# Kernel optimization log

Measured on AMD Instinct MI355X. Metric: run time of the kernel, lower is better.

The kernel has to match this reference:

```python
import jax, jax.numpy as jnp
import numpy as np

N_NODES = 50000
N_EDGES = 800000
F_IN = 128
HID = 128
HID4 = HID // 4  # 32
N_SEL = 8192


def gcn_conv(x, src, dst, norm, W, b, n_nodes):
    h = x @ W                              # [N, out]
    msg = h[src] * norm[:, None]           # gather + scale, [E+N, out]
    out = jax.ops.segment_sum(msg, dst, num_segments=n_nodes)  # scatter-add
    return out + b


def setup_inputs() -> dict:
    key = jax.random.key(0)
    ks = jax.random.split(key, 12)
    def glorot(k, shape):
        lim = np.sqrt(6.0 / (shape[0] + shape[1])).astype(np.float32)
        return jax.random.uniform(k, shape, jnp.float32, -lim, lim)
    return {
        "x": jax.random.normal(ks[0], (N_NODES, F_IN), jnp.float32),
        "edge_index": jax.random.randint(ks[1], (2, N_EDGES), 0, N_NODES, jnp.int64 if jax.config.jax_enable_x64 else jnp.int32),
        "relevant_batch_indices": jax.random.randint(ks[2], (N_SEL,), 0, N_NODES),
        "labels": jax.random.randint(ks[3], (N_SEL,), 0, 2),
        "W1": glorot(ks[4], (F_IN, HID)),   "b1": jnp.zeros((HID,), jnp.float32),
        "W2": glorot(ks[5], (HID, HID4)),   "b2": jnp.zeros((HID4,), jnp.float32),
        "W3": glorot(ks[6], (HID4, HID4)),  "b3": jnp.zeros((HID4,), jnp.float32),
        "Wl": glorot(ks[7], (HID4, 2)),     "bl": jnp.zeros((2,), jnp.float32),
    }


def reference(x, edge_index, relevant_batch_indices, labels, W1, b1, W2, b2, W3, b3, Wl, bl):
    n = x.shape[0]
    loops = jnp.arange(n, dtype=edge_index.dtype)
    src = jnp.concatenate([edge_index[0], loops])  # add self-loops
    dst = jnp.concatenate([edge_index[1], loops])
    deg = jax.ops.segment_sum(jnp.ones_like(dst, dtype=x.dtype), dst, num_segments=n)
    dis = jnp.where(deg > 0, jax.lax.rsqrt(jnp.maximum(deg, 1e-12)), 0.0)
    norm = dis[src] * dis[dst]             # [E+N]

    h = jax.nn.relu(gcn_conv(x, src, dst, norm, W1, b1, n))
    h = jax.nn.relu(gcn_conv(h, src, dst, norm, W2, b2, n))
    h = gcn_conv(h, src, dst, norm, W3, b3, n)

    logits = h[relevant_batch_indices] @ Wl + bl   # [N_SEL, 2]
    softmax_vals = jax.nn.softmax(logits, axis=1)
    lsm = jax.nn.log_softmax(logits, axis=1)
    # original slices lsm to labels length if longer; here shapes match
    lsm = lsm[: labels.shape[0]]
    return (lsm, softmax_vals)
```

## Files before the change

### kernel.cpp

```cpp
#include <hip/hip_runtime.h>
#include <hip/hip_fp16.h>

#define F_IN 128
#define HID 128
#define HID4 32
#define NPB 256
#define SRC_BITS 17
#define NBK 256
#define MAXBUCKET 256

static inline size_t alignup(size_t x) { return (x + 255) & ~(size_t)255; }

typedef _Float16 half8 __attribute__((ext_vector_type(8)));
typedef float f32x4 __attribute__((ext_vector_type(4)));

union F4H8 { float4 f; __half2 h[4]; };
union U2H4 { uint2 u; _Float16 h[4]; };
union UH2  { unsigned u; __half2 h; };


__global__ __launch_bounds__(1024) void hist_k(const int* __restrict__ dst,
                                               int* __restrict__ ghist,
                                               const float* __restrict__ W1,
                                               _Float16* __restrict__ Wt,
                                               int ne, int n_buckets) {
    __shared__ int h[MAXBUCKET];
    const int t = threadIdx.x;
    if (blockIdx.x < 16) {
        int q = blockIdx.x * 1024 + t;
        int k = q >> 7, n = q & 127;
        Wt[n * 128 + k] = (_Float16)W1[q];
    }
    for (int b = t; b < n_buckets; b += 1024) h[b] = 0;
    __syncthreads();
    const int chunk = (ne + NBK - 1) / NBK;
    const int beg = blockIdx.x * chunk;
    const int end = min(ne, beg + chunk);
    for (int e = beg + t; e < end; e += 1024)
        atomicAdd(&h[dst[e] / NPB], 1);
    __syncthreads();
    for (int b = t; b < n_buckets; b += 1024)
        ghist[(size_t)b * NBK + blockIdx.x] = h[b];
}


__global__ void scan_block_k(const int* __restrict__ in, int* __restrict__ out,
                             int* __restrict__ partials, int n) {
    __shared__ int tmp[256];
    int i = blockIdx.x * 256 + threadIdx.x;
    int v = (i < n) ? in[i] : 0;
    tmp[threadIdx.x] = v;
    __syncthreads();
    for (int off = 1; off < 256; off <<= 1) {
        int t = (threadIdx.x >= off) ? tmp[threadIdx.x - off] : 0;
        __syncthreads();
        tmp[threadIdx.x] += t;
        __syncthreads();
    }
    if (i < n) out[i] = tmp[threadIdx.x] - v;
    if (threadIdx.x == 255) partials[blockIdx.x] = tmp[255];
}

__global__ void scan_partials_k(int* __restrict__ partials, int nb) {
    __shared__ int tmp[256];
    int v = (threadIdx.x < nb) ? partials[threadIdx.x] : 0;
    tmp[threadIdx.x] = v;
    __syncthreads();
    for (int off = 1; off < 256; off <<= 1) {
        int t = (threadIdx.x >= off) ? tmp[threadIdx.x - off] : 0;
        __syncthreads();
        tmp[threadIdx.x] += t;
        __syncthreads();
    }
    if (threadIdx.x < nb) partials[threadIdx.x] = tmp[threadIdx.x] - v;
}


__global__ __launch_bounds__(1024) void scatter2_k(const int* __restrict__ src, const int* __restrict__ dst,
                                                   const int* __restrict__ goff,
                                                   const int* __restrict__ partial2,
                                                   unsigned* __restrict__ tmp, int ne, int n_buckets) {
    __shared__ int cur[MAXBUCKET];
    const int t = threadIdx.x;
    for (int b = t; b < n_buckets; b += 1024)
        cur[b] = goff[(size_t)b * NBK + blockIdx.x] + partial2[b];
    __syncthreads();
    const int chunk = (ne + NBK - 1) / NBK;
    const int beg = blockIdx.x * chunk;
    const int end = min(ne, beg + chunk);
    for (int e = beg + t; e < end; e += 1024) {
        int d = dst[e];
        int s = src[e];
        int pos = atomicAdd(&cur[d / NPB], 1);
        tmp[pos] = ((unsigned)(d & (NPB - 1)) << SRC_BITS) | (unsigned)s;
    }
}


__global__ __launch_bounds__(NPB) void binC_k(const unsigned* __restrict__ tmp,
                                              const int* __restrict__ goff,
                                              const int* __restrict__ partial2,
                                              int* __restrict__ deg, float* __restrict__ dis,
                                              int* __restrict__ rowoff, int* __restrict__ csr,
                                              int n_nodes, int ne, int n_buckets) {
    __shared__ int cnt[NPB];
    __shared__ int sc[NPB];
    const int t = threadIdx.x;
    const int bid = blockIdx.x;
    const int base = goff[(size_t)bid * NBK] + partial2[bid];
    const int end = (bid + 1 < n_buckets) ? goff[(size_t)(bid + 1) * NBK] + partial2[bid + 1] : ne;

    cnt[t] = 0;
    __syncthreads();
    for (int j = base + t; j < end; j += NPB)
        atomicAdd(&cnt[tmp[j] >> SRC_BITS], 1);
    __syncthreads();

    int mydeg = cnt[t];
    sc[t] = mydeg;
    __syncthreads();
    for (int off = 1; off < NPB; off <<= 1) {
        int v = (t >= off) ? sc[t - off] : 0;
        __syncthreads();
        sc[t] += v;
        __syncthreads();
    }
    int excl = sc[t] - mydeg;
    int node = bid * NPB + t;
    if (node < n_nodes) {
        deg[node] = mydeg;
        dis[node] = rsqrtf((float)(mydeg + 1));
        rowoff[node] = base + excl;
    }
    cnt[t] = base + excl;
    __syncthreads();
    for (int j = base + t; j < end; j += NPB) {
        unsigned e = tmp[j];
        int ld = e >> SRC_BITS;
        int s  = e & ((1u << SRC_BITS) - 1);
        int pos = atomicAdd(&cnt[ld], 1);
        csr[pos] = s;
    }
}


__global__ __launch_bounds__(256) void gemm1_mfma_k(const float* __restrict__ in,
                                                    const _Float16* __restrict__ Wt,
                                                    const float* __restrict__ dis,
                                                    __half* __restrict__ hout, int n_rows) {
    __shared__ _Float16 xs[64][136];
    const int t = threadIdx.x;
    const int row0 = blockIdx.x * 64;

    #pragma unroll
    for (int i = 0; i < 8; ++i) {
        int q = t + i * 256;
        int row = q >> 5, c4 = (q & 31) * 4;
        float4 v = make_float4(0.f, 0.f, 0.f, 0.f);
        if (row0 + row < n_rows) v = *(const float4*)(in + (size_t)(row0 + row) * 128 + c4);
        U2H4 cv;
        cv.h[0] = (_Float16)v.x; cv.h[1] = (_Float16)v.y;
        cv.h[2] = (_Float16)v.z; cv.h[3] = (_Float16)v.w;
        *(uint2*)&xs[row][c4] = cv.u;
    }
    __syncthreads();

    const int lane = t & 63;
    const int wave = t >> 6;
    const int r0 = wave * 16;
    const int lrow = lane & 15;
    const int kgrp = (lane >> 4) * 8;

    f32x4 acc[8];
    #pragma unroll
    for (int c = 0; c < 8; ++c) acc[c] = (f32x4){0.f, 0.f, 0.f, 0.f};

    #pragma unroll
    for (int kk = 0; kk < 4; ++kk) {
        const int k0 = kk * 32 + kgrp;
        half8 a = *(const half8*)&xs[r0 + lrow][k0];
        #pragma unroll
        for (int ct = 0; ct < 8; ++ct) {
            half8 b = *(const half8*)(Wt + (size_t)(ct * 16 + lrow) * 128 + k0);
            acc[ct] = __builtin_amdgcn_mfma_f32_16x16x32_f16(a, b, acc[ct], 0, 0, 0);
        }
    }

    const int rbase = row0 + r0 + (lane >> 4) * 4;
    #pragma unroll
    for (int i = 0; i < 4; ++i) {
        int row = rbase + i;
        if (row < n_rows) {
            float sc = dis[row];
            __half* p = hout + (size_t)row * 128 + lrow;
            #pragma unroll
            for (int ct = 0; ct < 8; ++ct)
                p[ct * 16] = __float2half(sc * acc[ct][i]);
        }
    }
}


__global__ void pull1_k(const __half* __restrict__ g, const int* __restrict__ rowoff,
                        const int* __restrict__ deg, const int* __restrict__ csr,
                        const float* __restrict__ dis, const float* __restrict__ b,
                        float* __restrict__ out, int n_nodes) {
    int gt = blockIdx.x * blockDim.x + threadIdx.x;
    int node = gt >> 4;
    int f0 = (gt & 15) * 8;
    if (node >= n_nodes) return;
    int beg = rowoff[node];
    int end = beg + deg[node];
    float dd = dis[node];

    float acc[8];
    {
        F4H8 v; v.f = *(const float4*)(g + (size_t)node * 128 + f0);
        #pragma unroll
        for (int k = 0; k < 4; ++k) {
            float2 p = __half22float2(v.h[k]);
            acc[2 * k] = p.x; acc[2 * k + 1] = p.y;
        }
    }

    int j = beg;
    for (; j + 2 <= end; j += 2) {
        int s0 = csr[j];
        int s1 = csr[j + 1];
        F4H8 v0; v0.f = *(const float4*)(g + (size_t)s0 * 128 + f0);
        F4H8 v1; v1.f = *(const float4*)(g + (size_t)s1 * 128 + f0);
        #pragma unroll
        for (int k = 0; k < 4; ++k) {
            float2 p0 = __half22float2(v0.h[k]);
            float2 p1 = __half22float2(v1.h[k]);
            acc[2 * k]     += p0.x + p1.x;
            acc[2 * k + 1] += p0.y + p1.y;
        }
    }
    if (j < end) {
        int s = csr[j];
        F4H8 v; v.f = *(const float4*)(g + (size_t)s * 128 + f0);
        #pragma unroll
        for (int k = 0; k < 4; ++k) {
            float2 p = __half22float2(v.h[k]);
            acc[2 * k] += p.x; acc[2 * k + 1] += p.y;
        }
    }

    float* o = out + (size_t)node * 128 + f0;
    float4 b0 = *(const float4*)(b + f0);
    float4 b1 = *(const float4*)(b + f0 + 4);
    *(float4*)o = make_float4(b0.x + dd * acc[0], b0.y + dd * acc[1],
                              b0.z + dd * acc[2], b0.w + dd * acc[3]);
    *(float4*)(o + 4) = make_float4(b1.x + dd * acc[4], b1.y + dd * acc[5],
                                    b1.z + dd * acc[6], b1.w + dd * acc[7]);
}


__global__ __launch_bounds__(256) void gemm2_k(const float* __restrict__ in,
                                               const float* __restrict__ W,
                                               const float* __restrict__ dis,
                                               __half* __restrict__ out, int n_rows) {
    __shared__ float xs[64][132];
    __shared__ float wt[128][32];
    const int t = threadIdx.x;
    const int row0 = blockIdx.x * 64;

    #pragma unroll
    for (int i = 0; i < 8; ++i) {
        int q = t + i * 256;
        int row = q >> 5, c4 = (q & 31) * 4;
        float4 v = make_float4(0.f, 0.f, 0.f, 0.f);
        if (row0 + row < n_rows) {
            v = *(const float4*)(in + (size_t)(row0 + row) * 128 + c4);
            v.x = fmaxf(v.x, 0.f); v.y = fmaxf(v.y, 0.f);
            v.z = fmaxf(v.z, 0.f); v.w = fmaxf(v.w, 0.f);
        }
        *(float4*)&xs[row][c4] = v;
    }
    #pragma unroll
    for (int i = 0; i < 4; ++i) {
        int q = t + i * 256;
        int kk = q >> 3, c4 = (q & 7) * 4;
        *(float4*)&wt[kk][c4] = *(const float4*)(W + (size_t)kk * 32 + c4);
    }
    __syncthreads();

    const int c4 = (t & 7) * 4;
    const int r2 = (t >> 3) * 2;

    float acc[2][4];
    #pragma unroll
    for (int i = 0; i < 2; ++i)
        #pragma unroll
        for (int j = 0; j < 4; ++j) acc[i][j] = 0.f;

    #pragma unroll 4
    for (int k = 0; k < 128; ++k) {
        float x0 = xs[r2][k], x1 = xs[r2 + 1][k];
        float4 w = *(float4*)&wt[k][c4];
        acc[0][0] += x0 * w.x; acc[0][1] += x0 * w.y; acc[0][2] += x0 * w.z; acc[0][3] += x0 * w.w;
        acc[1][0] += x1 * w.x; acc[1][1] += x1 * w.y; acc[1][2] += x1 * w.z; acc[1][3] += x1 * w.w;
    }

    #pragma unroll
    for (int i = 0; i < 2; ++i) {
        int row = row0 + r2 + i;
        if (row < n_rows) {
            float sc = dis[row];
            U2H4 cv;
            cv.h[0] = (_Float16)(sc * acc[i][0]);
            cv.h[1] = (_Float16)(sc * acc[i][1]);
            cv.h[2] = (_Float16)(sc * acc[i][2]);
            cv.h[3] = (_Float16)(sc * acc[i][3]);
            *(uint2*)(out + (size_t)row * 32 + c4) = cv.u;
        }
    }
}


__global__ void pull2_k(const __half* __restrict__ g, const int* __restrict__ rowoff,
                        const int* __restrict__ deg, const int* __restrict__ csr,
                        const float* __restrict__ dis, const float* __restrict__ b,
                        float* __restrict__ out, int n_nodes) {
    int gt = blockIdx.x * blockDim.x + threadIdx.x;
    int node = gt >> 3;
    int f0 = (gt & 7) * 4;
    if (node >= n_nodes) return;
    int beg = rowoff[node];
    int end = beg + deg[node];
    float dd = dis[node];

    float acc[4];
    {
        U2H4 v; v.u = *(const uint2*)(g + (size_t)node * 32 + f0);
        #pragma unroll
        for (int k = 0; k < 4; ++k) acc[k] = (float)v.h[k];
    }

    int j = beg;
    for (; j + 2 <= end; j += 2) {
        int s0 = csr[j];
        int s1 = csr[j + 1];
        U2H4 v0; v0.u = *(const uint2*)(g + (size_t)s0 * 32 + f0);
        U2H4 v1; v1.u = *(const uint2*)(g + (size_t)s1 * 32 + f0);
        #pragma unroll
        for (int k = 0; k < 4; ++k) acc[k] += (float)v0.h[k] + (float)v1.h[k];
    }
    if (j < end) {
        int s = csr[j];
        U2H4 v; v.u = *(const uint2*)(g + (size_t)s * 32 + f0);
        #pragma unroll
        for (int k = 0; k < 4; ++k) acc[k] += (float)v.h[k];
    }

    float4 bb = *(const float4*)(b + f0);
    *(float4*)(out + (size_t)node * 32 + f0) =
        make_float4(bb.x + dd * acc[0], bb.y + dd * acc[1],
                    bb.z + dd * acc[2], bb.w + dd * acc[3]);
}


__global__ __launch_bounds__(256) void gemm3_k(const float* __restrict__ in,
                                               const float* __restrict__ W,
                                               const float* __restrict__ dis,
                                               float* __restrict__ out, int n_rows) {
    __shared__ float xs[64][36];
    __shared__ float wt[32][32];
    const int t = threadIdx.x;
    const int row0 = blockIdx.x * 64;

    #pragma unroll
    for (int i = 0; i < 2; ++i) {
        int q = t + i * 256;
        int row = q >> 3, c4 = (q & 7) * 4;
        float4 v = make_float4(0.f, 0.f, 0.f, 0.f);
        if (row0 + row < n_rows) {
            v = *(const float4*)(in + (size_t)(row0 + row) * 32 + c4);
            v.x = fmaxf(v.x, 0.f); v.y = fmaxf(v.y, 0.f);
            v.z = fmaxf(v.z, 0.f); v.w = fmaxf(v.w, 0.f);
        }
        *(float4*)&xs[row][c4] = v;
    }
    {
        int kk = t >> 3, c4 = (t & 7) * 4;
        *(float4*)&wt[kk][c4] = *(const float4*)(W + (size_t)kk * 32 + c4);
    }
    __syncthreads();

    const int c4 = (t & 7) * 4;
    const int r2 = (t >> 3) * 2;

    float acc[2][4];
    #pragma unroll
    for (int i = 0; i < 2; ++i)
        #pragma unroll
        for (int j = 0; j < 4; ++j) acc[i][j] = 0.f;

    #pragma unroll
    for (int k = 0; k < 32; ++k) {
        float x0 = xs[r2][k], x1 = xs[r2 + 1][k];
        float4 w = *(float4*)&wt[k][c4];
        acc[0][0] += x0 * w.x; acc[0][1] += x0 * w.y; acc[0][2] += x0 * w.z; acc[0][3] += x0 * w.w;
        acc[1][0] += x1 * w.x; acc[1][1] += x1 * w.y; acc[1][2] += x1 * w.z; acc[1][3] += x1 * w.w;
    }

    #pragma unroll
    for (int i = 0; i < 2; ++i) {
        int row = row0 + r2 + i;
        if (row < n_rows) {
            float sc = dis[row];
            *(float4*)(out + (size_t)row * 32 + c4) =
                make_float4(sc * acc[i][0], sc * acc[i][1], sc * acc[i][2], sc * acc[i][3]);
        }
    }
}


__global__ void pull_head_k(const float* __restrict__ g, const int* __restrict__ rowoff,
                            const int* __restrict__ deg, const int* __restrict__ csr,
                            const float* __restrict__ dis, const float* __restrict__ b3,
                            const int* __restrict__ sel, const float* __restrict__ Wl,
                            const float* __restrict__ bl, float* __restrict__ out, int n_sel) {
    int gt = blockIdx.x * blockDim.x + threadIdx.x;
    int t = gt >> 3;
    int f0 = (gt & 7) * 4;
    if (t >= n_sel) return;
    int node = sel[t];
    int beg = rowoff[node];
    int end = beg + deg[node];
    float dd = dis[node];

    float4 acc = *(const float4*)(g + (size_t)node * 32 + f0);

    int j = beg;
    for (; j + 2 <= end; j += 2) {
        int s0 = csr[j];
        int s1 = csr[j + 1];
        float4 h0 = *(const float4*)(g + (size_t)s0 * 32 + f0);
        float4 h1 = *(const float4*)(g + (size_t)s1 * 32 + f0);
        acc.x += h0.x + h1.x;
        acc.y += h0.y + h1.y;
        acc.z += h0.z + h1.z;
        acc.w += h0.w + h1.w;
    }
    if (j < end) {
        int s = csr[j];
        float4 hs = *(const float4*)(g + (size_t)s * 32 + f0);
        acc.x += hs.x; acc.y += hs.y; acc.z += hs.z; acc.w += hs.w;
    }

    float4 bb = *(const float4*)(b3 + f0);
    float a0 = bb.x + dd * acc.x;
    float a1 = bb.y + dd * acc.y;
    float a2 = bb.z + dd * acc.z;
    float a3 = bb.w + dd * acc.w;

    float l0 = a0 * Wl[(f0 + 0) * 2] + a1 * Wl[(f0 + 1) * 2]
             + a2 * Wl[(f0 + 2) * 2] + a3 * Wl[(f0 + 3) * 2];
    float l1 = a0 * Wl[(f0 + 0) * 2 + 1] + a1 * Wl[(f0 + 1) * 2 + 1]
             + a2 * Wl[(f0 + 2) * 2 + 1] + a3 * Wl[(f0 + 3) * 2 + 1];
    #pragma unroll
    for (int m = 1; m < 8; m <<= 1) {
        l0 += __shfl_xor(l0, m);
        l1 += __shfl_xor(l1, m);
    }
    if ((gt & 7) == 0) {
        l0 += bl[0]; l1 += bl[1];
        float mx = fmaxf(l0, l1);
        float e0 = expf(l0 - mx), e1 = expf(l1 - mx);
        float s = e0 + e1;
        float ls = logf(s);
        *(float2*)(out + (size_t)t * 2) = make_float2((l0 - mx) - ls, (l1 - mx) - ls);
        *(float2*)(out + 2 * (size_t)n_sel + (size_t)t * 2) = make_float2(e0 / s, e1 / s);
    }
}


extern "C" void kernel_launch(void* const* d_in, const int* in_sizes, int n_in,
                              void* d_out, int out_size, void* d_ws, size_t ws_size,
                              hipStream_t stream) {
    const float* x  = (const float*)d_in[0];
    const int* edge = (const int*)d_in[1];
    const int* sel  = (const int*)d_in[2];
    const float* W1 = (const float*)d_in[4];
    const float* b1 = (const float*)d_in[5];
    const float* W2 = (const float*)d_in[6];
    const float* b2 = (const float*)d_in[7];
    const float* W3 = (const float*)d_in[8];
    const float* b3 = (const float*)d_in[9];
    const float* Wl = (const float*)d_in[10];
    const float* bl = (const float*)d_in[11];
    float* out = (float*)d_out;

    const int n_nodes = in_sizes[0] / F_IN;
    const int n_edges = in_sizes[1] / 2;
    const int n_sel   = in_sizes[2];
    const int* srcv = edge;
    const int* dstv = edge + n_edges;
    const int n_buckets = (n_nodes + NPB - 1) / NPB;
    const int n_gh = n_buckets * NBK;

    char* ws = (char*)d_ws;
    int*       deg      = (int*)ws;       ws += alignup((size_t)n_nodes * 4);
    float*     dis      = (float*)ws;     ws += alignup((size_t)n_nodes * 4);
    int*       rowoff   = (int*)ws;       ws += alignup((size_t)n_nodes * 4);
    int*       ghist    = (int*)ws;       ws += alignup((size_t)n_gh * 4);
    int*       goff     = (int*)ws;       ws += alignup((size_t)n_gh * 4);
    int*       partial2 = (int*)ws;       ws += alignup(1024);
    _Float16*  Wt       = (_Float16*)ws;  ws += alignup(128 * 128 * 2);
    unsigned*  tmp      = (unsigned*)ws;  ws += alignup((size_t)n_edges * 4);
    int*       csr      = (int*)ws;       ws += alignup((size_t)n_edges * 4);
    char*      bufA     = ws;             ws += alignup((size_t)n_nodes * HID * 4);
    float*     bufB     = (float*)ws;

    const int B = 256;
    #define GRD(n) (((n) + B - 1) / B)
    const int nblk2 = GRD(n_gh);

    hist_k<<<NBK, 1024, 0, stream>>>(dstv, ghist, W1, Wt, n_edges, n_buckets);
    scan_block_k<<<nblk2, B, 0, stream>>>(ghist, goff, partial2, n_gh);
    scan_partials_k<<<1, B, 0, stream>>>(partial2, nblk2);
    scatter2_k<<<NBK, 1024, 0, stream>>>(srcv, dstv, goff, partial2, tmp, n_edges, n_buckets);
    binC_k<<<n_buckets, NPB, 0, stream>>>(tmp, goff, partial2, deg, dis, rowoff, csr,
                                          n_nodes, n_edges, n_buckets);

    const int gemm_blocks = (n_nodes + 63) / 64;

    gemm1_mfma_k<<<gemm_blocks, B, 0, stream>>>(x, Wt, dis, (__half*)bufA, n_nodes);
    pull1_k<<<GRD(n_nodes * 16), B, 0, stream>>>((const __half*)bufA, rowoff, deg, csr, dis, b1, bufB, n_nodes);

    gemm2_k<<<gemm_blocks, B, 0, stream>>>(bufB, W2, dis, (__half*)bufA, n_nodes);
    pull2_k<<<GRD(n_nodes * 8), B, 0, stream>>>((const __half*)bufA, rowoff, deg, csr, dis, b2, bufB, n_nodes);

    gemm3_k<<<gemm_blocks, B, 0, stream>>>(bufB, W3, dis, (float*)bufA, n_nodes);
    pull_head_k<<<GRD(n_sel * 8), B, 0, stream>>>((const float*)bufA, rowoff, deg, csr, dis, b3,
                                                  sel, Wl, bl, out, n_sel);

    #undef GRD
}
```

Baseline: 139.1 us.

## Degree-sort nodes per bucket for pull kernels and store layer-1 output in fp16

binC_k now builds a per-bucket ordering of nodes grouped by in-degree, and pull1/pull2 take their node index from it, so threads in a wavefront handle nodes of similar degree and diverge less. The layer-1 pull output is also written as fp16 with ReLU applied, which halves the traffic written by pull1 and read by gemm2. This adds a small histogram and serial scan to binC, one extra indirection per pull thread, and less locality in the scattered output writes. It also adds fp16 rounding on the hidden activations.

```diff
diff --git a/kernel.cpp b/kernel.cpp
--- a/kernel.cpp
+++ b/kernel.cpp
@@ -16,7 +16,6 @@
 
 union F4H8 { float4 f; __half2 h[4]; };
 union U2H4 { uint2 u; _Float16 h[4]; };
-union UH2  { unsigned u; __half2 h; };
 
 
 __global__ __launch_bounds__(1024) void hist_k(const int* __restrict__ dst,
@@ -102,15 +101,19 @@
                                               const int* __restrict__ partial2,
                                               int* __restrict__ deg, float* __restrict__ dis,
                                               int* __restrict__ rowoff, int* __restrict__ csr,
+                                              int* __restrict__ order,
                                               int n_nodes, int ne, int n_buckets) {
     __shared__ int cnt[NPB];
     __shared__ int sc[NPB];
+    __shared__ int dh[64];
+    __shared__ int db[64];
     const int t = threadIdx.x;
     const int bid = blockIdx.x;
     const int base = goff[(size_t)bid * NBK] + partial2[bid];
     const int end = (bid + 1 < n_buckets) ? goff[(size_t)(bid + 1) * NBK] + partial2[bid + 1] : ne;
 
     cnt[t] = 0;
+    if (t < 64) dh[t] = 0;
     __syncthreads();
     for (int j = base + t; j < end; j += NPB)
         atomicAdd(&cnt[tmp[j] >> SRC_BITS], 1);
@@ -127,13 +130,28 @@
     }
     int excl = sc[t] - mydeg;
     int node = bid * NPB + t;
-    if (node < n_nodes) {
+    const bool valid = node < n_nodes;
+    if (valid) {
         deg[node] = mydeg;
         dis[node] = rsqrtf((float)(mydeg + 1));
         rowoff[node] = base + excl;
     }
     cnt[t] = base + excl;
-    __syncthreads();
+
+    int bin = min(mydeg, 63);
+    if (valid) atomicAdd(&dh[bin], 1);
+    __syncthreads();
+    if (t == 0) {
+        int run = 0;
+        #pragma unroll
+        for (int i = 0; i < 64; ++i) { db[i] = run; run += dh[i]; }
+    }
+    __syncthreads();
+    if (valid) {
+        int rank = atomicAdd(&db[bin], 1);
+        order[bid * NPB + rank] = node;
+    }
+
     for (int j = base + t; j < end; j += NPB) {
         unsigned e = tmp[j];
         int ld = e >> SRC_BITS;
@@ -203,12 +221,14 @@
 
 __global__ void pull1_k(const __half* __restrict__ g, const int* __restrict__ rowoff,
                         const int* __restrict__ deg, const int* __restrict__ csr,
+                        const int* __restrict__ order,
                         const float* __restrict__ dis, const float* __restrict__ b,
-                        float* __restrict__ out, int n_nodes) {
+                        __half* __restrict__ out, int n_nodes) {
     int gt = blockIdx.x * blockDim.x + threadIdx.x;
-    int node = gt >> 4;
+    int idx = gt >> 4;
     int f0 = (gt & 15) * 8;
-    if (node >= n_nodes) return;
+    if (idx >= n_nodes) return;
+    int node = order[idx];
     int beg = rowoff[node];
     int end = beg + deg[node];
     float dd = dis[node];
@@ -247,17 +267,18 @@
         }
     }
 
-    float* o = out + (size_t)node * 128 + f0;
     float4 b0 = *(const float4*)(b + f0);
     float4 b1 = *(const float4*)(b + f0 + 4);
-    *(float4*)o = make_float4(b0.x + dd * acc[0], b0.y + dd * acc[1],
-                              b0.z + dd * acc[2], b0.w + dd * acc[3]);
-    *(float4*)(o + 4) = make_float4(b1.x + dd * acc[4], b1.y + dd * acc[5],
-                                    b1.z + dd * acc[6], b1.w + dd * acc[7]);
-}
-
-
-__global__ __launch_bounds__(256) void gemm2_k(const float* __restrict__ in,
+    F4H8 o;
+    o.h[0] = __floats2half2_rn(fmaxf(b0.x + dd * acc[0], 0.f), fmaxf(b0.y + dd * acc[1], 0.f));
+    o.h[1] = __floats2half2_rn(fmaxf(b0.z + dd * acc[2], 0.f), fmaxf(b0.w + dd * acc[3], 0.f));
+    o.h[2] = __floats2half2_rn(fmaxf(b1.x + dd * acc[4], 0.f), fmaxf(b1.y + dd * acc[5], 0.f));
+    o.h[3] = __floats2half2_rn(fmaxf(b1.z + dd * acc[6], 0.f), fmaxf(b1.w + dd * acc[7], 0.f));
+    *(float4*)(out + (size_t)node * 128 + f0) = o.f;
+}
+
+
+__global__ __launch_bounds__(256) void gemm2_k(const __half* __restrict__ in,
                                                const float* __restrict__ W,
                                                const float* __restrict__ dis,
                                                __half* __restrict__ out, int n_rows) {
@@ -267,16 +288,19 @@
     const int row0 = blockIdx.x * 64;
 
     #pragma unroll
-    for (int i = 0; i < 8; ++i) {
+    for (int i = 0; i < 4; ++i) {
         int q = t + i * 256;
-        int row = q >> 5, c4 = (q & 31) * 4;
-        float4 v = make_float4(0.f, 0.f, 0.f, 0.f);
-        if (row0 + row < n_rows) {
-            v = *(const float4*)(in + (size_t)(row0 + row) * 128 + c4);
-            v.x = fmaxf(v.x, 0.f); v.y = fmaxf(v.y, 0.f);
-            v.z = fmaxf(v.z, 0.f); v.w = fmaxf(v.w, 0.f);
-        }
-        *(float4*)&xs[row][c4] = v;
+        int row = q >> 4, c8 = (q & 15) * 8;
+        F4H8 v;
+        v.f = make_float4(0.f, 0.f, 0.f, 0.f);
+        if (row0 + row < n_rows)
+            v.f = *(const float4*)(in + (size_t)(row0 + row) * 128 + c8);
+        #pragma unroll
+        for (int k = 0; k < 4; ++k) {
+            float2 p = __half22float2(v.h[k]);
+            xs[row][c8 + 2 * k] = p.x;
+            xs[row][c8 + 2 * k + 1] = p.y;
+        }
     }
     #pragma unroll
     for (int i = 0; i < 4; ++i) {
@@ -321,12 +345,14 @@
 
 __global__ void pull2_k(const __half* __restrict__ g, const int* __restrict__ rowoff,
                         const int* __restrict__ deg, const int* __restrict__ csr,
+                        const int* __restrict__ order,
                         const float* __restrict__ dis, const float* __restrict__ b,
                         float* __restrict__ out, int n_nodes) {
     int gt = blockIdx.x * blockDim.x + threadIdx.x;
-    int node = gt >> 3;
+    int idx = gt >> 3;
     int f0 = (gt & 7) * 4;
-    if (node >= n_nodes) return;
+    if (idx >= n_nodes) return;
+    int node = order[idx];
     int beg = rowoff[node];
     int end = beg + deg[node];
     float dd = dis[node];
@@ -505,6 +531,7 @@
     int*       deg      = (int*)ws;       ws += alignup((size_t)n_nodes * 4);
     float*     dis      = (float*)ws;     ws += alignup((size_t)n_nodes * 4);
     int*       rowoff   = (int*)ws;       ws += alignup((size_t)n_nodes * 4);
+    int*       order    = (int*)ws;       ws += alignup((size_t)n_nodes * 4);
     int*       ghist    = (int*)ws;       ws += alignup((size_t)n_gh * 4);
     int*       goff     = (int*)ws;       ws += alignup((size_t)n_gh * 4);
     int*       partial2 = (int*)ws;       ws += alignup(1024);
@@ -512,7 +539,7 @@
     unsigned*  tmp      = (unsigned*)ws;  ws += alignup((size_t)n_edges * 4);
     int*       csr      = (int*)ws;       ws += alignup((size_t)n_edges * 4);
     char*      bufA     = ws;             ws += alignup((size_t)n_nodes * HID * 4);
-    float*     bufB     = (float*)ws;
+    char*      bufB     = ws;
 
     const int B = 256;
     #define GRD(n) (((n) + B - 1) / B)
@@ -522,18 +549,20 @@
     scan_block_k<<<nblk2, B, 0, stream>>>(ghist, goff, partial2, n_gh);
     scan_partials_k<<<1, B, 0, stream>>>(partial2, nblk2);
     scatter2_k<<<NBK, 1024, 0, stream>>>(srcv, dstv, goff, partial2, tmp, n_edges, n_buckets);
-    binC_k<<<n_buckets, NPB, 0, stream>>>(tmp, goff, partial2, deg, dis, rowoff, csr,
+    binC_k<<<n_buckets, NPB, 0, stream>>>(tmp, goff, partial2, deg, dis, rowoff, csr, order,
                                           n_nodes, n_edges, n_buckets);
 
     const int gemm_blocks = (n_nodes + 63) / 64;
 
     gemm1_mfma_k<<<gemm_blocks, B, 0, stream>>>(x, Wt, dis, (__half*)bufA, n_nodes);
-    pull1_k<<<GRD(n_nodes * 16), B, 0, stream>>>((const __half*)bufA, rowoff, deg, csr, dis, b1, bufB, n_nodes);
-
-    gemm2_k<<<gemm_blocks, B, 0, stream>>>(bufB, W2, dis, (__half*)bufA, n_nodes);
-    pull2_k<<<GRD(n_nodes * 8), B, 0, stream>>>((const __half*)bufA, rowoff, deg, csr, dis, b2, bufB, n_nodes);
-
-    gemm3_k<<<gemm_blocks, B, 0, stream>>>(bufB, W3, dis, (float*)bufA, n_nodes);
+    pull1_k<<<GRD(n_nodes * 16), B, 0, stream>>>((const __half*)bufA, rowoff, deg, csr, order,
+                                                 dis, b1, (__half*)bufB, n_nodes);
+
+    gemm2_k<<<gemm_blocks, B, 0, stream>>>((const __half*)bufB, W2, dis, (__half*)bufA, n_nodes);
+    pull2_k<<<GRD(n_nodes * 8), B, 0, stream>>>((const __half*)bufA, rowoff, deg, csr, order,
+                                                dis, b2, (float*)bufB, n_nodes);
+
+    gemm3_k<<<gemm_blocks, B, 0, stream>>>((const float*)bufB, W3, dis, (float*)bufA, n_nodes);
     pull_head_k<<<GRD(n_sel * 8), B, 0, stream>>>((const float*)bufA, rowoff, deg, csr, dis, b3,
                                                   sel, Wl, bl, out, n_sel);
 
```

After: 141.5 us. No clear change (+1.8%).
